# Optimization experiments

Measured on AMD Instinct MI355X. Metric: run time of the kernel, lower is better.

Reference implementation:

```python
import jax, jax.numpy as jnp
import numpy as np

VOCAB = 30522
EMB = 128
H = 128          # per-direction GRU hidden (text_hidden_size // 2)
TXT = 256        # text_hidden_size
VDIM = 1024      # visual_feature_dim
VHID = 256       # video_hidden_dim
ADIM = 256       # alignment_dim
REG = 0.05
N_ITERS = 10


def gru_seq(x, Wi, Wh, bi, bh):
    """PyTorch-convention GRU. x:(B,T,I), Wi:(3H,I), Wh:(3H,H). Returns (B,T,H)."""
    B, T, _ = x.shape
    Hd = Wh.shape[1]
    xg = jnp.einsum('bti,gi->btg', x, Wi) + bi  # precompute input gates (B,T,3H)

    def step(h, xg_t):
        hg = h @ Wh.T + bh
        xr, xz, xn = jnp.split(xg_t, 3, axis=-1)
        hr, hz, hn = jnp.split(hg, 3, axis=-1)
        r = jax.nn.sigmoid(xr + hr)
        z = jax.nn.sigmoid(xz + hz)
        n = jnp.tanh(xn + r * hn)
        h_new = (1.0 - z) * n + z * h
        return h_new, h_new

    h0 = jnp.zeros((B, Hd), x.dtype)
    _, hs = jax.lax.scan(step, h0, jnp.swapaxes(xg, 0, 1))
    return jnp.swapaxes(hs, 0, 1)


def mlp_scorer(x, W1, b1, w2, b2, act):
    h = act(jnp.einsum('bsd,hd->bsh', x, W1) + b1)
    return jax.nn.sigmoid(jnp.einsum('bsh,h->bs', h, w2) + b2)


def sinkhorn(E, V, reg=REG, num_iters=N_ITERS):
    B, K, _ = E.shape
    M = V.shape[1]
    En = E / (jnp.linalg.norm(E, axis=-1, keepdims=True) + 1e-12)
    Vn = V / (jnp.linalg.norm(V, axis=-1, keepdims=True) + 1e-12)
    C = 1.0 - jnp.einsum('bkd,bmd->bkm', En, Vn)
    Km = jnp.exp(-C / reg)
    mu = jnp.full((B, K), 1.0 / K, E.dtype)
    nu = jnp.full((B, M), 1.0 / M, E.dtype)
    u = jnp.full((B, K), 1.0 / K, E.dtype)
    v = jnp.full((B, M), 1.0 / M, E.dtype)
    for _ in range(num_iters):
        u = mu / (jnp.einsum('bkm,bm->bk', Km, v) + 1e-8)
        v = nu / (jnp.einsum('bkm,bk->bm', Km, u) + 1e-8)
    T = u[:, :, None] * Km * v[:, None, :]
    dist = jnp.sum(T * C) / B
    return dist, T


def setup_inputs() -> dict:
    key = jax.random.key(0)
    ks = jax.random.split(key, 24)
    B, S, W, M = 16, 128, 32, 256
    s = 0.02
    inp = {
        'input_ids': jax.random.randint(ks[0], (B, S, W), 0, VOCAB),
        'attention_mask': jnp.ones((B, S, W), jnp.int64 if jax.config.jax_enable_x64 else jnp.int32),
        'video_features': jax.random.normal(ks[1], (B, M, VDIM), jnp.float32),
        'emb': jax.random.normal(ks[2], (VOCAB, EMB), jnp.float32) * s,
        'gru_Wi_f': jax.random.normal(ks[3], (3 * H, EMB), jnp.float32) * s,
        'gru_Wh_f': jax.random.normal(ks[4], (3 * H, H), jnp.float32) * s,
        'gru_bi_f': jnp.zeros((3 * H,), jnp.float32),
        'gru_bh_f': jnp.zeros((3 * H,), jnp.float32),
        'gru_Wi_b': jax.random.normal(ks[5], (3 * H, EMB), jnp.float32) * s,
        'gru_Wh_b': jax.random.normal(ks[6], (3 * H, H), jnp.float32) * s,
        'gru_bi_b': jnp.zeros((3 * H,), jnp.float32),
        'gru_bh_b': jnp.zeros((3 * H,), jnp.float32),
        'tproj_W': jax.random.normal(ks[7], (ADIM, TXT), jnp.float32) * s,
        'tproj_b': jnp.zeros((ADIM,), jnp.float32),
        'vproj_W': jax.random.normal(ks[8], (ADIM, VDIM), jnp.float32) * s,
        'vproj_b': jnp.zeros((ADIM,), jnp.float32),
        'tsum_W1': jax.random.normal(ks[9], (H, TXT), jnp.float32) * s,
        'tsum_b1': jnp.zeros((H,), jnp.float32),
        'tsum_w2': jax.random.normal(ks[10], (H,), jnp.float32) * s,
        'tsum_b2': jnp.zeros((), jnp.float32),
        'vsum_W1': jax.random.normal(ks[11], (VHID, VDIM), jnp.float32) * s,
        'vsum_b1': jnp.zeros((VHID,), jnp.float32),
        'vsum_w2': jax.random.normal(ks[12], (VHID,), jnp.float32) * s,
        'vsum_b2': jnp.zeros((), jnp.float32),
        'vts_W1': jax.random.normal(ks[13], (VHID, VDIM), jnp.float32) * s,
        'vts_b1': jnp.zeros((VHID,), jnp.float32),
        'vts_w2': jax.random.normal(ks[14], (VHID,), jnp.float32) * s,
        'vts_b2': jnp.zeros((), jnp.float32),
    }
    return inp


def reference(input_ids, attention_mask, video_features, emb,
              gru_Wi_f, gru_Wh_f, gru_bi_f, gru_bh_f,
              gru_Wi_b, gru_Wh_b, gru_bi_b, gru_bh_b,
              tproj_W, tproj_b, vproj_W, vproj_b,
              tsum_W1, tsum_b1, tsum_w2, tsum_b2,
              vsum_W1, vsum_b1, vsum_w2, vsum_b2,
              vts_W1, vts_b1, vts_w2, vts_b2):
    B, S, W = input_ids.shape
    flat = input_ids.reshape(B * S, W)
    embeds = emb[flat]  # (B*S, W, EMB); padding_idx=0 row is just a table row here
    fwd = gru_seq(embeds, gru_Wi_f, gru_Wh_f, gru_bi_f, gru_bh_f)
    bwd = gru_seq(embeds[:, ::-1, :], gru_Wi_b, gru_Wh_b, gru_bi_b, gru_bh_b)[:, ::-1, :]
    gru_out = jnp.concatenate([fwd, bwd], axis=-1)  # (B*S, W, 2H)
    text_features = gru_out.mean(axis=1).reshape(B, S, TXT)

    text_seg_probs = jnp.zeros((B, S), text_features.dtype)
    video_seg_probs = mlp_scorer(video_features, vts_W1, vts_b1, vts_w2, vts_b2, jax.nn.relu)
    text_summ_probs = mlp_scorer(text_features, tsum_W1, tsum_b1, tsum_w2, tsum_b2, jnp.tanh)
    video_summ_probs = mlp_scorer(video_features, vsum_W1, vsum_b1, vsum_w2, vsum_b2, jnp.tanh)

    E_w = text_features * text_summ_probs[:, :, None]
    V_w = video_features * video_summ_probs[:, :, None]
    E_proj = jnp.einsum('bsd,ad->bsa', E_w, tproj_W) + tproj_b
    V_proj = jnp.einsum('bmd,ad->bma', V_w, vproj_W) + vproj_b

    ot_loss, T = sinkhorn(E_proj, V_proj)
    return (text_seg_probs, text_features, video_seg_probs, text_summ_probs,
            video_summ_probs, ot_loss, T)
```

## Files before the change

kernel.cpp:

```cpp
#include <hip/hip_runtime.h>
#include <hip/hip_bf16.h>

typedef unsigned short u16;
typedef __attribute__((ext_vector_type(8))) short short8;
typedef __attribute__((ext_vector_type(4))) float f32x4;

static __device__ __forceinline__ float bf2f(u16 x) {
    unsigned int u = ((unsigned int)x) << 16;
    return __uint_as_float(u);
}
static __device__ __forceinline__ u16 f2bf(float f) {
    unsigned int u = __float_as_uint(f);
    unsigned int r = (u + 0x7fffu + ((u >> 16) & 1u)) >> 16;
    return (u16)r;
}
static __device__ __forceinline__ float sigmoidf(float x) {
    return 1.0f / (1.0f + expf(-x));
}
static __device__ __forceinline__ float fsig(float x) {
    return __fdividef(1.0f, 1.0f + __expf(-x));
}
static __device__ __forceinline__ float ftanh(float x) {
    return 1.0f - __fdividef(2.0f, 1.0f + __expf(2.0f * x));
}

__global__ void k_zero(float* __restrict__ out) {
    int t = blockIdx.x * 256 + threadIdx.x;
    if (t < 2048) out[t] = 0.0f;
    if (t == 0) out[536576] = 0.0f;
}

__global__ void k_cvte(const float* __restrict__ emb, const float* __restrict__ WiF,
                       const float* __restrict__ WiB, u16* __restrict__ dst) {
    long i4 = ((long)blockIdx.x * 256 + threadIdx.x) * 4;
    if (i4 >= 4005120) return;
    float4 v;
    if (i4 < 3906816) v = *(const float4*)(emb + i4);
    else if (i4 < 3955968) v = *(const float4*)(WiF + (i4 - 3906816));
    else v = *(const float4*)(WiB + (i4 - 3955968));
    ushort4 o;
    o.x = f2bf(v.x); o.y = f2bf(v.y); o.z = f2bf(v.z); o.w = f2bf(v.w);
    *(ushort4*)(dst + i4) = o;
}

__global__ __launch_bounds__(256) void k_xg2(const int* __restrict__ ids, const u16* __restrict__ embb,
                                             const u16* __restrict__ Wib, const float* __restrict__ bi,
                                             u16* __restrict__ xgt) {
    __shared__ u16 As[128][40];
    __shared__ u16 Bs[128][40];
    const int t = threadIdx.x;
    const int m0 = blockIdx.x * 128, n0 = blockIdx.y * 128;
    const int w = t >> 6, l = t & 63;
    const int wr = w >> 1, wc = w & 1;
    const int lrow = l & 15, lk = (l >> 4) * 8;
    f32x4 acc[4][4] = {};
#pragma unroll
    for (int kk = 0; kk < 4; kk++) {
        const int k0 = kk * 32;
        int4 ra[2], rb[2];
#pragma unroll
        for (int it = 0; it < 2; it++) {
            int e = it * 256 + t;
            int row = e >> 2, c8 = (e & 3) * 8;
            int id = ids[m0 + row];
            ra[it] = *(const int4*)(embb + (long)id * 128 + k0 + c8);
            rb[it] = *(const int4*)(Wib + (long)(n0 + row) * 128 + k0 + c8);
        }
        __syncthreads();
#pragma unroll
        for (int it = 0; it < 2; it++) {
            int e = it * 256 + t;
            int row = e >> 2, c8 = (e & 3) * 8;
            *(int4*)&As[row][c8] = ra[it];
            *(int4*)&Bs[row][c8] = rb[it];
        }
        __syncthreads();
        short8 af[4], bf[4];
#pragma unroll
        for (int f = 0; f < 4; f++) {
            af[f] = *(const short8*)&As[wr * 64 + f * 16 + lrow][lk];
            bf[f] = *(const short8*)&Bs[wc * 64 + f * 16 + lrow][lk];
        }
#pragma unroll
        for (int fm = 0; fm < 4; fm++)
#pragma unroll
            for (int fn = 0; fn < 4; fn++)
                acc[fm][fn] = __builtin_amdgcn_mfma_f32_16x16x32_bf16(af[fm], bf[fn], acc[fm][fn], 0, 0, 0);
    }
    const int orow = (l >> 4) * 4, ocol = l & 15;
#pragma unroll
    for (int fm = 0; fm < 4; fm++)
#pragma unroll
        for (int fn = 0; fn < 4; fn++) {
            const int col = n0 + wc * 64 + fn * 16 + ocol;
            const float bbv = bi[col];
            const int row0 = m0 + wr * 64 + fm * 16 + orow;
#pragma unroll
            for (int r = 0; r < 4; r++) {
                const int mrow = row0 + r;
                xgt[((long)(mrow & 31) * 2048 + (mrow >> 5)) * 384 + col]
                    = f2bf(acc[fm][fn][r] + bbv);
            }
        }
}

__global__ __launch_bounds__(512) void k_scan3(const u16* __restrict__ xgt,
                                               const float* __restrict__ Wh,
                                               const float* __restrict__ bh,
                                               float* __restrict__ tf_out, int dir) {
    __shared__ u16 hbuf[2][16][140];
    __shared__ u16 xbuf[2][8][392];
    const int t = threadIdx.x;
    const int w = t >> 6, l = t & 63;
    const int lr = l & 15, hi = l >> 4;
    const int seq0 = blockIdx.x * 8;

    short8 breg[3][4];
    float bb[3];
#pragma unroll
    for (int g = 0; g < 3; g++) {
        const int ncol = g * 128 + w * 16 + lr;
        const float* wrow = Wh + (long)ncol * 128;
        bb[g] = bh[ncol];
#pragma unroll
        for (int q = 0; q < 4; q++) {
            float4 a = *(const float4*)(wrow + q * 32 + hi * 8);
            float4 b = *(const float4*)(wrow + q * 32 + hi * 8 + 4);
            short8 s;
            s[0] = f2bf(a.x); s[1] = f2bf(a.y); s[2] = f2bf(a.z); s[3] = f2bf(a.w);
            s[4] = f2bf(b.x); s[5] = f2bf(b.y); s[6] = f2bf(b.z); s[7] = f2bf(b.w);
            breg[g][q] = s;
        }
    }
    for (int i = t; i < 2240; i += 512) ((int*)hbuf)[i] = 0;
    const int seqr = t / 48, part = t % 48;
    if (t < 384) {
        const int tp0 = dir ? 31 : 0;
        *(int4*)&xbuf[0][seqr][part * 8] =
            *(const int4*)(xgt + ((long)tp0 * 2048 + seq0 + seqr) * 384 + part * 8);
    }
    float hreg[4] = {0.f, 0.f, 0.f, 0.f};
    float macc[4] = {0.f, 0.f, 0.f, 0.f};
    __syncthreads();

    for (int tt = 0; tt < 32; tt++) {
        const int cur = tt & 1;
        int4 pre;
        const bool do_pre = (tt < 31) && (t < 384);
        if (do_pre) {
            const int tpn = dir ? (30 - tt) : (tt + 1);
            pre = *(const int4*)(xgt + ((long)tpn * 2048 + seq0 + seqr) * 384 + part * 8);
        }
        short8 af[4];
#pragma unroll
        for (int q = 0; q < 4; q++)
            af[q] = *(const short8*)&hbuf[cur][lr][q * 32 + hi * 8];
        f32x4 acc[3];
#pragma unroll
        for (int g = 0; g < 3; g++) {
            f32x4 a = {0.f, 0.f, 0.f, 0.f};
#pragma unroll
            for (int q = 0; q < 4; q++)
                a = __builtin_amdgcn_mfma_f32_16x16x32_bf16(af[q], breg[g][q], a, 0, 0, 0);
            acc[g] = a;
        }
        if (hi < 2) {
            const int c = w * 16 + lr;
#pragma unroll
            for (int r = 0; r < 4; r++) {
                const int m = hi * 4 + r;
                float xr = bf2f(xbuf[cur][m][c]);
                float xz = bf2f(xbuf[cur][m][128 + c]);
                float xn = bf2f(xbuf[cur][m][256 + c]);
                float rg = fsig(xr + acc[0][r] + bb[0]);
                float zg = fsig(xz + acc[1][r] + bb[1]);
                float ng = ftanh(xn + rg * (acc[2][r] + bb[2]));
                float h = (1.0f - zg) * ng + zg * hreg[r];
                hreg[r] = h;
                macc[r] += h;
                hbuf[cur ^ 1][m][c] = f2bf(h);
            }
        }
        if (do_pre) *(int4*)&xbuf[cur ^ 1][seqr][part * 8] = pre;
        __syncthreads();
    }

    if (hi < 2) {
#pragma unroll
        for (int r = 0; r < 4; r++)
            tf_out[(long)(seq0 + hi * 4 + r) * 256 + dir * 128 + w * 16 + lr]
                = macc[r] * (1.0f / 32.0f);
    }
}

__global__ void k_tsum(const float* __restrict__ tf, const float* __restrict__ W1,
                       const float* __restrict__ b1, const float* __restrict__ w2,
                       const float* __restrict__ b2, float* __restrict__ out) {
    __shared__ float x[256];
    __shared__ float wsum[2];
    const int row = blockIdx.x, t = threadIdx.x;
    x[t] = tf[(long)row * 256 + t];
    x[t + 128] = tf[(long)row * 256 + 128 + t];
    __syncthreads();
    float acc = 0.f;
    const float* w = W1 + (long)t * 256;
#pragma unroll 8
    for (int i = 0; i < 256; i += 4) {
        float4 w4 = *(const float4*)(w + i);
        acc += w4.x * x[i] + w4.y * x[i + 1] + w4.z * x[i + 2] + w4.w * x[i + 3];
    }
    float h = ftanh(acc + b1[t]) * w2[t];
    for (int o = 32; o > 0; o >>= 1) h += __shfl_xor(h, o);
    if ((t & 63) == 0) wsum[t >> 6] = h;
    __syncthreads();
    if (t == 0) out[row] = fsig(wsum[0] + wsum[1] + b2[0]);
}

__global__ void k_cvt(const float* __restrict__ vf, const float* __restrict__ wa,
                      const float* __restrict__ wb2, const float* __restrict__ wc2,
                      u16* __restrict__ Xb, u16* __restrict__ Wb) {
    long gid = (long)blockIdx.x * 256 + threadIdx.x;
    long i4 = gid * 4;
    float4 v;
    u16* dst;
    if (i4 < 4194304) {
        v = *(const float4*)(vf + i4);
        dst = Xb + i4;
    } else {
        long j = i4 - 4194304;
        dst = Wb + j;
        if (j < 262144) v = *(const float4*)(wa + j);
        else if (j < 524288) v = *(const float4*)(wb2 + (j - 262144));
        else v = *(const float4*)(wc2 + (j - 524288));
    }
    ushort4 o;
    o.x = f2bf(v.x); o.y = f2bf(v.y); o.z = f2bf(v.z); o.w = f2bf(v.w);
    *(ushort4*)dst = o;
}

__global__ __launch_bounds__(256) void k_gemmv(const u16* __restrict__ Xb, const u16* __restrict__ Wb,
                                               float* __restrict__ G) {
    __shared__ u16 As[128][40];
    __shared__ u16 Bs[128][40];
    const int t = threadIdx.x;
    const int m0 = blockIdx.x * 128, n0 = blockIdx.y * 128;
    const int w = t >> 6, l = t & 63;
    const int wr = w >> 1, wc = w & 1;
    const int lrow = l & 15, lk = (l >> 4) * 8;
    f32x4 acc[4][4] = {};
    for (int kk = 0; kk < 32; kk++) {
        const int k0 = kk * 32;
        int4 ra[2], rb[2];
#pragma unroll
        for (int it = 0; it < 2; it++) {
            int e = it * 256 + t;
            int row = e >> 2, c8 = (e & 3) * 8;
            ra[it] = *(const int4*)(Xb + (long)(m0 + row) * 1024 + k0 + c8);
            rb[it] = *(const int4*)(Wb + (long)(n0 + row) * 1024 + k0 + c8);
        }
        __syncthreads();
#pragma unroll
        for (int it = 0; it < 2; it++) {
            int e = it * 256 + t;
            int row = e >> 2, c8 = (e & 3) * 8;
            *(int4*)&As[row][c8] = ra[it];
            *(int4*)&Bs[row][c8] = rb[it];
        }
        __syncthreads();
        short8 af[4], bf[4];
#pragma unroll
        for (int f = 0; f < 4; f++) {
            af[f] = *(const short8*)&As[wr * 64 + f * 16 + lrow][lk];
            bf[f] = *(const short8*)&Bs[wc * 64 + f * 16 + lrow][lk];
        }
#pragma unroll
        for (int fm = 0; fm < 4; fm++)
#pragma unroll
            for (int fn = 0; fn < 4; fn++)
                acc[fm][fn] = __builtin_amdgcn_mfma_f32_16x16x32_bf16(af[fm], bf[fn], acc[fm][fn], 0, 0, 0);
    }
    const int orow = (l >> 4) * 4, ocol = l & 15;
#pragma unroll
    for (int fm = 0; fm < 4; fm++)
#pragma unroll
        for (int fn = 0; fn < 4; fn++) {
            long base = (long)(m0 + wr * 64 + fm * 16 + orow) * 768 + n0 + wc * 64 + fn * 16 + ocol;
#pragma unroll
            for (int r = 0; r < 4; r++)
                G[base + (long)r * 768] = acc[fm][fn][r];
        }
}

__global__ void k_vepi(const float* __restrict__ G,
                       const float* __restrict__ bv, const float* __restrict__ w2v, const float* __restrict__ b2v,
                       const float* __restrict__ bt, const float* __restrict__ w2t, const float* __restrict__ b2t,
                       const float* __restrict__ vpb,
                       float* __restrict__ V, float* __restrict__ vsp, float* __restrict__ vseg) {
    const int r = blockIdx.x * 4 + (threadIdx.x >> 6);
    const int lane = threadIdx.x & 63;
    const float* g = G + (long)r * 768;
    float s1 = 0.f, s2 = 0.f;
#pragma unroll
    for (int c = 0; c < 4; c++) {
        int h = lane + c * 64;
        s1 += ftanh(g[h] + bv[h]) * w2v[h];
        s2 += fmaxf(g[256 + h] + bt[h], 0.0f) * w2t[h];
    }
    for (int o = 32; o > 0; o >>= 1) { s1 += __shfl_xor(s1, o); s2 += __shfl_xor(s2, o); }
    float p = fsig(s1 + b2v[0]);
    if (lane == 0) {
        vsp[r] = p;
        vseg[r] = fsig(s2 + b2t[0]);
    }
#pragma unroll
    for (int c = 0; c < 4; c++) {
        int a = lane + c * 64;
        V[(long)r * 256 + a] = vpb[a] + p * g[512 + a];
    }
}

__global__ void k_eproj(const float* __restrict__ tf, const float* __restrict__ tsp,
                        const float* __restrict__ W, const float* __restrict__ b,
                        float* __restrict__ E) {
    __shared__ float x[8][256];
    __shared__ float p[8];
    const int r0 = blockIdx.x * 8, t = threadIdx.x;
    const float4* src = (const float4*)(tf + (long)r0 * 256);
    for (int i = t; i < 512; i += 256) ((float4*)&x[0][0])[i] = src[i];
    if (t < 8) p[t] = tsp[r0 + t];
    __syncthreads();
    float acc[8] = {};
    const float* w = W + (long)t * 256;
    for (int i = 0; i < 256; i += 4) {
        float4 w4 = *(const float4*)(w + i);
#pragma unroll
        for (int r = 0; r < 8; r++) {
            float4 x4 = *(const float4*)&x[r][i];
            acc[r] += w4.x * x4.x + w4.y * x4.y + w4.z * x4.z + w4.w * x4.w;
        }
    }
    const float bb = b[t];
#pragma unroll
    for (int r = 0; r < 8; r++) E[(long)(r0 + r) * 256 + t] = bb + p[r] * acc[r];
}

__global__ void k_norm(float* __restrict__ E, float* __restrict__ V) {
    const int w = threadIdx.x >> 6, lane = threadIdx.x & 63;
    const int row = blockIdx.x * 4 + w;
    float* ptr = (row < 2048) ? (E + (long)row * 256) : (V + (long)(row - 2048) * 256);
    float4 v = ((float4*)ptr)[lane];
    float s = v.x * v.x + v.y * v.y + v.z * v.z + v.w * v.w;
    for (int o = 32; o > 0; o >>= 1) s += __shfl_xor(s, o);
    float sc = 1.0f / (sqrtf(s) + 1e-12f);
    v.x *= sc; v.y *= sc; v.z *= sc; v.w *= sc;
    ((float4*)ptr)[lane] = v;
}

__global__ void k_cost(const float* __restrict__ E, const float* __restrict__ V,
                       float* __restrict__ C, float* __restrict__ Km) {
    __shared__ float en[16][256];
    const int b = blockIdx.x, k0 = blockIdx.y * 16, t = threadIdx.x;
    const float4* esrc = (const float4*)(E + ((long)b * 128 + k0) * 256);
    for (int i = t; i < 1024; i += 256) ((float4*)&en[0][0])[i] = esrc[i];
    __syncthreads();
    float acc[16] = {};
    const float* vrow = V + ((long)b * 256 + t) * 256;
    for (int i = 0; i < 256; i += 4) {
        float4 v4 = *(const float4*)(vrow + i);
#pragma unroll
        for (int k = 0; k < 16; k++) {
            float4 e4 = *(const float4*)&en[k][i];
            acc[k] += e4.x * v4.x + e4.y * v4.y + e4.z * v4.z + e4.w * v4.w;
        }
    }
#pragma unroll
    for (int k = 0; k < 16; k++) {
        float c = 1.0f - acc[k];
        long idx = (long)b * 32768 + (long)(k0 + k) * 256 + t;
        C[idx] = c;
        Km[idx] = __expf(-20.0f * c);
    }
}

__global__ void k_sink(const float* __restrict__ C, const float* __restrict__ Km,
                       float* __restrict__ T, float* __restrict__ loss) {
    __shared__ float u[128];
    __shared__ float v[256];
    __shared__ float red[8];
    const int b = blockIdx.x, t = threadIdx.x;
    const float* Kb = Km + (long)b * 32768;
    const float* Cb = C + (long)b * 32768;
    if (t < 128) u[t] = 1.0f / 128.0f;
    if (t < 256) v[t] = 1.0f / 256.0f;
    __syncthreads();
    for (int it = 0; it < 10; it++) {
        {
            const int k = t >> 2, q = t & 3;
            const float* kr = Kb + (long)k * 256 + q * 64;
            float s = 0.f;
#pragma unroll 4
            for (int m = 0; m < 64; m += 4) {
                float4 k4 = *(const float4*)(kr + m);
                float4 vv = *(const float4*)&v[q * 64 + m];
                s += k4.x * vv.x + k4.y * vv.y + k4.z * vv.z + k4.w * vv.w;
            }
            s += __shfl_xor(s, 1);
            s += __shfl_xor(s, 2);
            float un = (1.0f / 128.0f) / (s + 1e-8f);
            u[k] = un;
            __syncthreads();
        }
        {
            const int m = t >> 1, q = t & 1;
            float s = 0.f;
            for (int k = 0; k < 64; k += 4) {
                float4 u4 = *(const float4*)&u[q * 64 + k];
                s += Kb[(long)(q * 64 + k + 0) * 256 + m] * u4.x;
                s += Kb[(long)(q * 64 + k + 1) * 256 + m] * u4.y;
                s += Kb[(long)(q * 64 + k + 2) * 256 + m] * u4.z;
                s += Kb[(long)(q * 64 + k + 3) * 256 + m] * u4.w;
            }
            s += __shfl_xor(s, 1);
            float vn = (1.0f / 256.0f) / (s + 1e-8f);
            v[m] = vn;
            __syncthreads();
        }
    }
    float part = 0.f;
    for (int i = 0; i < 64; i++) {
        int idx = i * 512 + t;
        int k = idx >> 8, m = idx & 255;
        float tv = u[k] * Kb[idx] * v[m];
        T[(long)b * 32768 + idx] = tv;
        part += tv * Cb[idx];
    }
    for (int o = 32; o > 0; o >>= 1) part += __shfl_xor(part, o);
    if ((t & 63) == 0) red[t >> 6] = part;
    __syncthreads();
    if (t == 0) {
        float s = red[0] + red[1] + red[2] + red[3] + red[4] + red[5] + red[6] + red[7];
        atomicAdd(loss, s * (1.0f / 16.0f));
    }
}

extern "C" void kernel_launch(void* const* d_in, const int* in_sizes, int n_in,
                              void* d_out, int out_size, void* d_ws, size_t ws_size,
                              hipStream_t stream) {
    const int*   ids  = (const int*)d_in[0];
    const float* vf   = (const float*)d_in[2];
    const float* emb  = (const float*)d_in[3];
    const float* WiF  = (const float*)d_in[4];
    const float* WhF  = (const float*)d_in[5];
    const float* biF  = (const float*)d_in[6];
    const float* bhF  = (const float*)d_in[7];
    const float* WiB  = (const float*)d_in[8];
    const float* WhB  = (const float*)d_in[9];
    const float* biB  = (const float*)d_in[10];
    const float* bhB  = (const float*)d_in[11];
    const float* tpW  = (const float*)d_in[12];
    const float* tpb  = (const float*)d_in[13];
    const float* vpW  = (const float*)d_in[14];
    const float* vpb  = (const float*)d_in[15];
    const float* tsW1 = (const float*)d_in[16];
    const float* tsb1 = (const float*)d_in[17];
    const float* tsw2 = (const float*)d_in[18];
    const float* tsb2 = (const float*)d_in[19];
    const float* vsW1 = (const float*)d_in[20];
    const float* vsb1 = (const float*)d_in[21];
    const float* vsw2 = (const float*)d_in[22];
    const float* vsb2 = (const float*)d_in[23];
    const float* vtW1 = (const float*)d_in[24];
    const float* vtb1 = (const float*)d_in[25];
    const float* vtw2 = (const float*)d_in[26];
    const float* vtb2 = (const float*)d_in[27];
    float* out = (float*)d_out;

    char* ws = (char*)d_ws;
    u16*   XGT = (u16*)ws;
    u16*   Xb = (u16*)ws;
    u16*   Wb = (u16*)(ws + 8388608);
    float* G  = (float*)(ws + 9961472);
    u16*   embb = (u16*)(ws + 50331648);
    u16*   WibF = embb + 3906816;
    u16*   WibB = embb + 3955968;
    float* E  = (float*)(ws + 50331648);
    float* V  = (float*)(ws + 52428800);
    float* C  = (float*)(ws + 56623104);
    float* Km = (float*)(ws + 58720256);

    float* tf   = out + 2048;
    float* vseg = out + 526336;
    float* tsp  = out + 530432;
    float* vsp  = out + 532480;
    float* loss = out + 536576;
    float* T    = out + 536577;

    k_zero<<<8, 256, 0, stream>>>(out);

    k_cvte<<<3912, 256, 0, stream>>>(emb, WiF, WiB, embb);
    k_xg2<<<dim3(512, 3), 256, 0, stream>>>(ids, embb, WibF, biF, XGT);
    k_scan3<<<256, 512, 0, stream>>>(XGT, WhF, bhF, tf, 0);
    k_xg2<<<dim3(512, 3), 256, 0, stream>>>(ids, embb, WibB, biB, XGT);
    k_scan3<<<256, 512, 0, stream>>>(XGT, WhB, bhB, tf, 1);

    k_cvt<<<4864, 256, 0, stream>>>(vf, vsW1, vtW1, vpW, Xb, Wb);
    k_gemmv<<<dim3(32, 6), 256, 0, stream>>>(Xb, Wb, G);
    k_vepi<<<1024, 256, 0, stream>>>(G, vsb1, vsw2, vsb2, vtb1, vtw2, vtb2, vpb, V, vsp, vseg);

    k_tsum<<<2048, 128, 0, stream>>>(tf, tsW1, tsb1, tsw2, tsb2, tsp);
    k_eproj<<<256, 256, 0, stream>>>(tf, tsp, tpW, tpb, E);
    k_norm<<<1536, 256, 0, stream>>>(E, V);
    k_cost<<<dim3(16, 8), 256, 0, stream>>>(E, V, C, Km);
    k_sink<<<16, 512, 0, stream>>>(C, Km, T, loss);
}
```

Baseline: 510.2 us.

## Double-buffer video GEMM tiles and split Sinkhorn into LDS-resident iterations plus wide output pass

The video GEMM now prefetches the next K-slice into registers while MFMAs run on the current LDS buffer. Its shared tiles are double-buffered in a k-quad-major layout, which cuts the loop to one barrier per step. The Sinkhorn kernel first loads each batch's 128x256 kernel matrix into LDS (128 KB) so all ten iterations read from shared memory instead of global. The final transport plan and loss are moved to a separate 256-block kernel so the output writes use many CUs instead of 16. The large LDS footprint limits occupancy to one block per CU, and the extra launch adds a small fixed cost.

```diff
diff --git a/kernel.cpp b/kernel.cpp
--- a/kernel.cpp
+++ b/kernel.cpp
@@ -13,9 +13,6 @@
     unsigned int u = __float_as_uint(f);
     unsigned int r = (u + 0x7fffu + ((u >> 16) & 1u)) >> 16;
     return (u16)r;
-}
-static __device__ __forceinline__ float sigmoidf(float x) {
-    return 1.0f / (1.0f + expf(-x));
 }
 static __device__ __forceinline__ float fsig(float x) {
     return __fdividef(1.0f, 1.0f + __expf(-x));
@@ -240,44 +237,60 @@
 
 __global__ __launch_bounds__(256) void k_gemmv(const u16* __restrict__ Xb, const u16* __restrict__ Wb,
                                                float* __restrict__ G) {
-    __shared__ u16 As[128][40];
-    __shared__ u16 Bs[128][40];
+    __shared__ u16 As[2][4][130][8];
+    __shared__ u16 Bs[2][4][130][8];
     const int t = threadIdx.x;
     const int m0 = blockIdx.x * 128, n0 = blockIdx.y * 128;
     const int w = t >> 6, l = t & 63;
     const int wr = w >> 1, wc = w & 1;
-    const int lrow = l & 15, lk = (l >> 4) * 8;
+    const int lrow = l & 15, lq = l >> 4;
+    const int ldr = t >> 2, ldq = t & 3;
     f32x4 acc[4][4] = {};
+    int4 ra[2], rb[2];
+#pragma unroll
+    for (int it = 0; it < 2; it++) {
+        int row = ldr + it * 64;
+        ra[it] = *(const int4*)(Xb + (long)(m0 + row) * 1024 + ldq * 8);
+        rb[it] = *(const int4*)(Wb + (long)(n0 + row) * 1024 + ldq * 8);
+    }
+#pragma unroll
+    for (int it = 0; it < 2; it++) {
+        int row = ldr + it * 64;
+        *(int4*)&As[0][ldq][row][0] = ra[it];
+        *(int4*)&Bs[0][ldq][row][0] = rb[it];
+    }
+    __syncthreads();
     for (int kk = 0; kk < 32; kk++) {
-        const int k0 = kk * 32;
-        int4 ra[2], rb[2];
-#pragma unroll
-        for (int it = 0; it < 2; it++) {
-            int e = it * 256 + t;
-            int row = e >> 2, c8 = (e & 3) * 8;
-            ra[it] = *(const int4*)(Xb + (long)(m0 + row) * 1024 + k0 + c8);
-            rb[it] = *(const int4*)(Wb + (long)(n0 + row) * 1024 + k0 + c8);
-        }
-        __syncthreads();
-#pragma unroll
-        for (int it = 0; it < 2; it++) {
-            int e = it * 256 + t;
-            int row = e >> 2, c8 = (e & 3) * 8;
-            *(int4*)&As[row][c8] = ra[it];
-            *(int4*)&Bs[row][c8] = rb[it];
-        }
-        __syncthreads();
+        const int cur = kk & 1;
+        if (kk < 31) {
+            const int k0 = (kk + 1) * 32;
+#pragma unroll
+            for (int it = 0; it < 2; it++) {
+                int row = ldr + it * 64;
+                ra[it] = *(const int4*)(Xb + (long)(m0 + row) * 1024 + k0 + ldq * 8);
+                rb[it] = *(const int4*)(Wb + (long)(n0 + row) * 1024 + k0 + ldq * 8);
+            }
+        }
         short8 af[4], bf[4];
 #pragma unroll
         for (int f = 0; f < 4; f++) {
-            af[f] = *(const short8*)&As[wr * 64 + f * 16 + lrow][lk];
-            bf[f] = *(const short8*)&Bs[wc * 64 + f * 16 + lrow][lk];
+            af[f] = *(const short8*)&As[cur][lq][wr * 64 + f * 16 + lrow][0];
+            bf[f] = *(const short8*)&Bs[cur][lq][wc * 64 + f * 16 + lrow][0];
         }
 #pragma unroll
         for (int fm = 0; fm < 4; fm++)
 #pragma unroll
             for (int fn = 0; fn < 4; fn++)
                 acc[fm][fn] = __builtin_amdgcn_mfma_f32_16x16x32_bf16(af[fm], bf[fn], acc[fm][fn], 0, 0, 0);
+        if (kk < 31) {
+#pragma unroll
+            for (int it = 0; it < 2; it++) {
+                int row = ldr + it * 64;
+                *(int4*)&As[cur ^ 1][ldq][row][0] = ra[it];
+                *(int4*)&Bs[cur ^ 1][ldq][row][0] = rb[it];
+            }
+        }
+        __syncthreads();
     }
     const int orow = (l >> 4) * 4, ocol = l & 15;
 #pragma unroll
@@ -382,21 +395,21 @@
     }
 }
 
-__global__ void k_sink(const float* __restrict__ C, const float* __restrict__ Km,
-                       float* __restrict__ T, float* __restrict__ loss) {
+__global__ __launch_bounds__(512) void k_sink2(const float* __restrict__ Km, float* __restrict__ UV) {
+    __shared__ float Kl[128][256];
     __shared__ float u[128];
     __shared__ float v[256];
-    __shared__ float red[8];
     const int b = blockIdx.x, t = threadIdx.x;
     const float* Kb = Km + (long)b * 32768;
-    const float* Cb = C + (long)b * 32768;
+    for (int i = t; i < 8192; i += 512)
+        ((float4*)&Kl[0][0])[i] = ((const float4*)Kb)[i];
     if (t < 128) u[t] = 1.0f / 128.0f;
     if (t < 256) v[t] = 1.0f / 256.0f;
     __syncthreads();
     for (int it = 0; it < 10; it++) {
         {
             const int k = t >> 2, q = t & 3;
-            const float* kr = Kb + (long)k * 256 + q * 64;
+            const float* kr = &Kl[k][q * 64];
             float s = 0.f;
 #pragma unroll 4
             for (int m = 0; m < 64; m += 4) {
@@ -415,10 +428,10 @@
             float s = 0.f;
             for (int k = 0; k < 64; k += 4) {
                 float4 u4 = *(const float4*)&u[q * 64 + k];
-                s += Kb[(long)(q * 64 + k + 0) * 256 + m] * u4.x;
-                s += Kb[(long)(q * 64 + k + 1) * 256 + m] * u4.y;
-                s += Kb[(long)(q * 64 + k + 2) * 256 + m] * u4.z;
-                s += Kb[(long)(q * 64 + k + 3) * 256 + m] * u4.w;
+                s += Kl[q * 64 + k + 0][m] * u4.x;
+                s += Kl[q * 64 + k + 1][m] * u4.y;
+                s += Kl[q * 64 + k + 2][m] * u4.z;
+                s += Kl[q * 64 + k + 3][m] * u4.w;
             }
             s += __shfl_xor(s, 1);
             float vn = (1.0f / 256.0f) / (s + 1e-8f);
@@ -426,21 +439,33 @@
             __syncthreads();
         }
     }
+    if (t < 128) UV[b * 384 + t] = u[t];
+    if (t < 256) UV[b * 384 + 128 + t] = v[t];
+}
+
+__global__ void k_tout(const float* __restrict__ C, const float* __restrict__ Km,
+                       const float* __restrict__ UV, float* __restrict__ T,
+                       float* __restrict__ loss) {
+    __shared__ float red[4];
+    const int b = blockIdx.x >> 4, kc = blockIdx.x & 15;
+    const int t = threadIdx.x;
+    const float* Kb = Km + (long)b * 32768;
+    const float* Cb = C + (long)b * 32768;
+    const float vv = UV[b * 384 + 128 + t];
     float part = 0.f;
-    for (int i = 0; i < 64; i++) {
-        int idx = i * 512 + t;
-        int k = idx >> 8, m = idx & 255;
-        float tv = u[k] * Kb[idx] * v[m];
+#pragma unroll
+    for (int i = 0; i < 8; i++) {
+        const int k = kc * 8 + i;
+        const float uu = UV[b * 384 + k];
+        const long idx = (long)k * 256 + t;
+        float tv = uu * Kb[idx] * vv;
         T[(long)b * 32768 + idx] = tv;
         part += tv * Cb[idx];
     }
     for (int o = 32; o > 0; o >>= 1) part += __shfl_xor(part, o);
     if ((t & 63) == 0) red[t >> 6] = part;
     __syncthreads();
-    if (t == 0) {
-        float s = red[0] + red[1] + red[2] + red[3] + red[4] + red[5] + red[6] + red[7];
-        atomicAdd(loss, s * (1.0f / 16.0f));
-    }
+    if (t == 0) atomicAdd(loss, (red[0] + red[1] + red[2] + red[3]) * (1.0f / 16.0f));
 }
 
 extern "C" void kernel_launch(void* const* d_in, const int* in_sizes, int n_in,
@@ -480,6 +505,7 @@
     u16*   Xb = (u16*)ws;
     u16*   Wb = (u16*)(ws + 8388608);
     float* G  = (float*)(ws + 9961472);
+    float* UVb = (float*)(ws + 9961472);
     u16*   embb = (u16*)(ws + 50331648);
     u16*   WibF = embb + 3906816;
     u16*   WibB = embb + 3955968;
@@ -511,5 +537,6 @@
     k_eproj<<<256, 256, 0, stream>>>(tf, tsp, tpW, tpb, E);
     k_norm<<<1536, 256, 0, stream>>>(E, V);
     k_cost<<<dim3(16, 8), 256, 0, stream>>>(E, V, C, Km);
-    k_sink<<<16, 512, 0, stream>>>(C, Km, T, loss);
-}
+    k_sink2<<<16, 512, 0, stream>>>(Km, UVb);
+    k_tout<<<256, 256, 0, stream>>>(C, Km, UVb, T, loss);
+}
```

Result: faster. 495.6 us (-2.9%).
